# Optimization experiments

Measured on AMD Instinct MI355X. Metric: run time of the kernel, lower is better.

The kernel has to match this reference:

```python
import jax, jax.numpy as jnp
import numpy as np
from jax import lax

B, C, H0, W0 = 8, 128, 62, 62
G, K, DIL, STRIDE, PAD = 4, 3, 1, 1, 1
P = K * K
GC = C // G
OFFSET_SCALE = 1.0


def setup_inputs() -> dict:
    key = jax.random.key(0)
    ks = jax.random.split(key, 10)
    s = 0.05
    return {
        "x": jax.random.normal(ks[0], (B, C, H0, W0), jnp.float32),
        "conv_w": jax.random.normal(ks[1], (C, C, 1, 1), jnp.float32) * s,
        "conv_b": jax.random.normal(ks[2], (C,), jnp.float32) * s,
        "in_proj_w": jax.random.normal(ks[3], (C, C), jnp.float32) * s,
        "in_proj_b": jnp.zeros((C,), jnp.float32),
        "dw_w": jax.random.normal(ks[4], (C, 1, K, K), jnp.float32) * s,
        "dw_b": jnp.zeros((C,), jnp.float32),
        "ln_g": jnp.ones((C,), jnp.float32),
        "ln_b": jnp.zeros((C,), jnp.float32),
        "off_w": jax.random.normal(ks[5], (C, G * P * 2), jnp.float32) * s,
        "off_b": jax.random.normal(ks[6], (G * P * 2,), jnp.float32) * s,
        "mask_w": jax.random.normal(ks[7], (C, G * P), jnp.float32) * s,
        "mask_b": jnp.zeros((G * P,), jnp.float32),
        "out_proj_w": jax.random.normal(ks[8], (C, C), jnp.float32) * s,
        "out_proj_b": jnp.zeros((C,), jnp.float32),
    }


def _bilinear_sample(img, ix, iy, Hp, Wp):
    # img: [B, G, Hp*Wp, GC] flattened spatial; ix, iy: [B, G, Q, P] pixel coords.
    # Matches torch grid_sample(bilinear, zeros, align_corners=False).
    x0 = jnp.floor(ix)
    y0 = jnp.floor(iy)

    def gather(xi, yi):
        valid = (xi >= 0) & (xi <= Wp - 1) & (yi >= 0) & (yi <= Hp - 1)
        xc = jnp.clip(xi, 0, Wp - 1).astype(jnp.int32)
        yc = jnp.clip(yi, 0, Hp - 1).astype(jnp.int32)
        lin = (yc * Wp + xc).reshape(img.shape[0], img.shape[1], -1)  # [B,G,Q*P]
        v = jnp.take_along_axis(img, lin[..., None], axis=2)          # [B,G,Q*P,GC]
        v = v.reshape(xi.shape + (img.shape[-1],))
        return v * valid[..., None].astype(img.dtype)

    wx1 = (ix - x0)[..., None]
    wx0 = 1.0 - wx1
    wy1 = (iy - y0)[..., None]
    wy0 = 1.0 - wy1
    return (gather(x0, y0) * wx0 * wy0
            + gather(x0 + 1.0, y0) * wx1 * wy0
            + gather(x0, y0 + 1.0) * wx0 * wy1
            + gather(x0 + 1.0, y0 + 1.0) * wx1 * wy1)


def _dcnv3_core(x_proj, offset, mask):
    # x_proj: [B,H,W,C] NHWC; offset: [B,H,W,G*P*2]; mask: [B,H,W,G*P] (softmaxed)
    Bn, H, W, _ = x_proj.shape
    xp = jnp.pad(x_proj, ((0, 0), (PAD, PAD), (PAD, PAD), (0, 0)))
    Hp, Wp = H + 2 * PAD, W + 2 * PAD  # H_out == H for K=3, PAD=1, STRIDE=1
    # reference points (normalized to padded size)
    ref_x = (jnp.arange(W, dtype=jnp.float32) * STRIDE + (DIL * (K - 1)) / 2.0 + 0.5) / Wp
    ref_y = (jnp.arange(H, dtype=jnp.float32) * STRIDE + (DIL * (K - 1)) / 2.0 + 0.5) / Hp
    ref = jnp.stack(jnp.broadcast_arrays(ref_x[None, :], ref_y[:, None]), -1)  # [H,W,2] (x,y)
    # dilation grid (same ordering as torch.meshgrid(x_lin, y_lin))
    klin = (jnp.arange(K, dtype=jnp.float32) * DIL - (DIL * (K - 1)) // 2)
    gx, gy = jnp.meshgrid(klin, klin, indexing='ij')
    grid = jnp.stack([gx / Wp, gy / Hp], -1).reshape(P, 2)
    grid = jnp.tile(grid[None], (G, 1, 1)).reshape(G * P, 2)
    spatial_norm = jnp.array([Wp, Hp], jnp.float32)
    loc = (ref[:, :, None, :] + grid[None, None] * OFFSET_SCALE)[None] \
        + offset.reshape(Bn, H, W, G * P, 2) * OFFSET_SCALE / spatial_norm
    g = 2.0 * loc - 1.0  # normalized grid in [-1,1]
    ix = ((g[..., 0] + 1.0) * Wp - 1.0) / 2.0  # align_corners=False unnormalize
    iy = ((g[..., 1] + 1.0) * Hp - 1.0) / 2.0
    Q = H * W
    ix = ix.reshape(Bn, Q, G, P).transpose(0, 2, 1, 3)  # [B,G,Q,P]
    iy = iy.reshape(Bn, Q, G, P).transpose(0, 2, 1, 3)
    img = xp.reshape(Bn, Hp * Wp, G, GC).transpose(0, 2, 1, 3)  # [B,G,S,GC]
    sampled = _bilinear_sample(img, ix, iy, Hp, Wp)             # [B,G,Q,P,GC]
    m = mask.reshape(Bn, Q, G, P).transpose(0, 2, 1, 3)
    out = jnp.einsum('bgqpc,bgqp->bqgc', sampled, m)
    return out.reshape(Bn, H, W, G * GC)


def reference(x, conv_w, conv_b, in_proj_w, in_proj_b, dw_w, dw_b, ln_g, ln_b,
              off_w, off_b, mask_w, mask_b, out_proj_w, out_proj_b):
    dn = ('NCHW', 'OIHW', 'NCHW')
    # 1x1 conv with padding=1 (spatial grows by 2 on each dim)
    y = lax.conv_general_dilated(x, conv_w, (1, 1), ((PAD, PAD), (PAD, PAD)),
                                 dimension_numbers=dn) + conv_b[None, :, None, None]
    t = y.transpose(0, 2, 3, 1)  # NHWC
    x_proj = t @ in_proj_w + in_proj_b
    # offset/mask branch: depthwise conv + LayerNorm + GELU
    d = lax.conv_general_dilated(y, dw_w, (1, 1), ((1, 1), (1, 1)),
                                 dimension_numbers=dn,
                                 feature_group_count=C) + dw_b[None, :, None, None]
    d = d.transpose(0, 2, 3, 1)
    mu = d.mean(-1, keepdims=True)
    var = ((d - mu) ** 2).mean(-1, keepdims=True)
    d = (d - mu) / jnp.sqrt(var + 1e-5) * ln_g + ln_b
    d = jax.nn.gelu(d, approximate=False)
    offset = d @ off_w + off_b
    Bn, H, W, _ = d.shape
    m = jax.nn.softmax((d @ mask_w + mask_b).reshape(Bn, H, W, G, P), axis=-1)
    out = _dcnv3_core(x_proj, offset, m.reshape(Bn, H, W, G * P))
    out = out @ out_proj_w + out_proj_b
    return out.transpose(0, 3, 1, 2)  # back to NCHW
```

## Files before the change

kernel.cpp:

```cpp
#include <hip/hip_runtime.h>
#include <math.h>

#define BB 8
#define CH 128
#define HH 64
#define WWID 64
#define HIN 62
#define WIN 62
#define SPIN (HIN*WIN)
#define HP 66
#define WP 66
#define GP2 70
#define GG 4
#define GCH 32
#define NPIX (BB*HH*WWID)
#define ASTRIDE 136
#define XPHALFS ((size_t)BB*GP2*GP2*CH)

typedef _Float16 v8h __attribute__((ext_vector_type(8)));
typedef _Float16 v4h __attribute__((ext_vector_type(4)));
typedef float    v4f __attribute__((ext_vector_type(4)));
typedef float    f4a __attribute__((ext_vector_type(4), aligned(4)));

__device__ inline int xcd_swizzle(int bid, int nblk8) {
    return (bid & 7) * nblk8 + (bid >> 3);
}

__global__ __launch_bounds__(256) void p0_pack(const float* __restrict__ conv_w,
                                               const float* __restrict__ in_proj_w,
                                               const float* __restrict__ off_w,
                                               const float* __restrict__ mask_w,
                                               const float* __restrict__ out_proj_w,
                                               const float* __restrict__ dw_w,
                                               _Float16* __restrict__ wp,
                                               float* __restrict__ dwT,
                                               _Float16* __restrict__ xpad16) {
    int t = threadIdx.x;
    int blk = blockIdx.x;
    if (blk >= 32) {
        size_t nvec = XPHALFS / 8;
        for (size_t i = (size_t)(blk - 32) * 256 + t; i < nvec; i += 32 * 256)
            *(v8h*)&xpad16[i * 8] = (v8h)(_Float16)0;
        return;
    }
    if (blk == 31) {
        if (t < 128) {
            #pragma unroll
            for (int tap = 0; tap < 9; tap++) dwT[tap * 128 + t] = dw_w[t * 9 + tap];
        }
        return;
    }
    int tid = blk * 256 + t;
    int mat, base;
    if (tid < 2048)      { mat = 0; base = 0; }
    else if (tid < 4096) { mat = 1; base = 2048; }
    else if (tid < 5888) { mat = 2; base = 4096; }
    else                 { mat = 3; base = 5888; }
    int fi = tid - base;
    int nt = fi >> 8, rem = fi & 255, kc = rem >> 6, lane = rem & 63;
    int n = nt * 16 + (lane & 15);
    int kbase = kc * 32 + ((lane >> 4) & 3) * 8;
    _Float16* dst = wp + (size_t)tid * 8;
    #pragma unroll
    for (int j = 0; j < 8; j++) {
        int k = kbase + j;
        float v;
        if (mat == 0)      v = conv_w[n * CH + k];
        else if (mat == 1) v = in_proj_w[k * CH + n];
        else if (mat == 2) v = (n < 72) ? off_w[k * 72 + n]
                               : (n < 108 ? mask_w[k * 36 + (n - 72)] : 0.f);
        else               v = out_proj_w[k * CH + n];
        dst[j] = (_Float16)v;
    }
}

__device__ inline void mfma_loop8(const _Float16* __restrict__ a16,
                                  const _Float16* __restrict__ wp,
                                  v4f acc[4], int t) {
    int lane = t & 63;
    int wv = t >> 6;
    int mt = wv >> 1, ntb = (wv & 1) * 4;
    const _Float16* abase = a16 + (mt * 16 + (lane & 15)) * ASTRIDE + ((lane >> 4) * 8);
    #pragma unroll
    for (int kc = 0; kc < 4; kc++) {
        v8h av = *(const v8h*)(abase + kc * 32);
        #pragma unroll
        for (int j = 0; j < 4; j++) {
            v8h bv = *(const v8h*)(wp + ((size_t)((ntb + j) * 4 + kc) * 64 + lane) * 8);
            acc[j] = __builtin_amdgcn_mfma_f32_16x16x32_f16(av, bv, acc[j], 0, 0, 0);
        }
    }
}

__device__ inline void acc_to_a16_8(_Float16* a16, v4f acc[4], int t) {
    int lane = t & 63, ncol = lane & 15;
    int wv = t >> 6;
    int m0 = (wv >> 1) * 16 + ((lane >> 4) * 4);
    int ntb = (wv & 1) * 4;
    #pragma unroll
    for (int j = 0; j < 4; j++)
        #pragma unroll
        for (int r = 0; r < 4; r++)
            a16[(m0 + r) * ASTRIDE + (ntb + j) * 16 + ncol] = (_Float16)acc[j][r];
}

__global__ __launch_bounds__(256) void gA_conv_inproj(const float* __restrict__ x,
                                                      const _Float16* __restrict__ wp_conv,
                                                      const _Float16* __restrict__ wp_in,
                                                      const float* __restrict__ conv_b,
                                                      const float* __restrict__ in_b,
                                                      _Float16* __restrict__ y16,
                                                      _Float16* __restrict__ xpad16) {
    __shared__ _Float16 a16[32 * ASTRIDE];
    int eff = xcd_swizzle(blockIdx.x, 128);
    int pix0 = eff * 32;
    int t = threadIdx.x;
    int h = (pix0 >> 6) & 63, b = pix0 >> 12, wb = pix0 & 63;
    bool hin = (h >= 1 && h <= 62);
    for (int q = t; q < 1024; q += 256) {
        int c = q >> 3, w4l = (q & 7) * 4;
        int w4 = wb + w4l;
        float4 v = make_float4(0.f, 0.f, 0.f, 0.f);
        if (hin) {
            const float* xr = x + ((size_t)(b * CH + c)) * SPIN + (h - 1) * WIN;
            if (w4 == 0)       { f4a e = *(const f4a*)&xr[0];      v = make_float4(0.f, e[0], e[1], e[2]); }
            else if (w4 == 60) { f4a e = *(const f4a*)&xr[58];     v = make_float4(e[1], e[2], e[3], 0.f); }
            else               { f4a e = *(const f4a*)&xr[w4 - 1]; v = make_float4(e[0], e[1], e[2], e[3]); }
        }
        a16[(w4l + 0) * ASTRIDE + c] = (_Float16)v.x;
        a16[(w4l + 1) * ASTRIDE + c] = (_Float16)v.y;
        a16[(w4l + 2) * ASTRIDE + c] = (_Float16)v.z;
        a16[(w4l + 3) * ASTRIDE + c] = (_Float16)v.w;
    }
    __syncthreads();
    int lane = t & 63, ncol = lane & 15;
    int ntb = ((t >> 6) & 1) * 4;
    v4f acc[4];
    #pragma unroll
    for (int j = 0; j < 4; j++) {
        float bv = conv_b[(ntb + j) * 16 + ncol];
        acc[j] = (v4f){bv, bv, bv, bv};
    }
    mfma_loop8(a16, wp_conv, acc, t);
    __syncthreads();
    acc_to_a16_8(a16, acc, t);
    __syncthreads();
    {
        _Float16* dst = y16 + (size_t)pix0 * CH;
        for (int q = t; q < 512; q += 256)
            *(v8h*)&dst[q * 8] = *(const v8h*)&a16[(q >> 4) * ASTRIDE + (q & 15) * 8];
    }
    v4f acc2[4];
    #pragma unroll
    for (int j = 0; j < 4; j++) {
        float bv = in_b[(ntb + j) * 16 + ncol];
        acc2[j] = (v4f){bv, bv, bv, bv};
    }
    mfma_loop8(a16, wp_in, acc2, t);
    __syncthreads();
    acc_to_a16_8(a16, acc2, t);
    __syncthreads();
    {
        _Float16* dst = xpad16 + (size_t)(((b * GP2) + h + 3) * GP2 + 3 + wb) * CH;
        for (int q = t; q < 512; q += 256)
            *(v8h*)&dst[q * 8] = *(const v8h*)&a16[(q >> 4) * ASTRIDE + (q & 15) * 8];
    }
}

__global__ __launch_bounds__(512) void gF_dwln_offmask(const _Float16* __restrict__ y16,
                                                       const _Float16* __restrict__ wp_om,
                                                       const float* __restrict__ dwT,
                                                       const float* __restrict__ dw_b,
                                                       const float* __restrict__ ln_g,
                                                       const float* __restrict__ ln_b,
                                                       const float* __restrict__ off_b,
                                                       const float* __restrict__ mask_b,
                                                       float* __restrict__ tapmeta) {
    __shared__ char smem[49920];
    _Float16* ylds = (_Float16*)smem;
    int t = threadIdx.x;
    int eff = xcd_swizzle(blockIdx.x, 64);
    int pix0 = eff * 64;
    int h = (pix0 >> 6) & 63, b = pix0 >> 12;
    if (h == 0 || h == 63) {
        for (int i = t; i < 3120; i += 512) *(v8h*)&ylds[i * 8] = (v8h)(_Float16)0;
        __syncthreads();
    }
    for (int idx = t; idx < 3072; idx += 512) {
        int r = idx >> 10, w = (idx >> 4) & 63, c8 = idx & 15;
        int hh = h + r - 1;
        if (hh >= 0 && hh <= 63) {
            v8h v = *(const v8h*)&y16[(size_t)(((b * 64 + hh) * 64 + w) * CH) + c8 * 8];
            *(v8h*)&ylds[(size_t)((r * 16 + c8) * 65 + w) * 8] = v;
        }
    }
    __syncthreads();
    int px = t >> 3, q8 = t & 7;
    float acc[16];
    #pragma unroll
    for (int cb = 0; cb < 4; cb++) *(float4*)&acc[cb * 4] = *(const float4*)&dw_b[q8 * 16 + cb * 4];
    #pragma unroll
    for (int r = 0; r < 3; r++) {
        #pragma unroll
        for (int kx = 0; kx < 3; kx++) {
            int wq = px + kx - 1;
            bool valid = (wq >= 0 && wq <= 63);
            int wpc = min(max(wq, 0), 63);
            int tap = r * 3 + kx;
            if (valid) {
                #pragma unroll
                for (int cb = 0; cb < 2; cb++) {
                    v8h yv = *(const v8h*)&ylds[(size_t)((r * 16 + q8 * 2 + cb) * 65 + wpc) * 8];
                    float4 wa = *(const float4*)&dwT[tap * 128 + q8 * 16 + cb * 8];
                    float4 wb = *(const float4*)&dwT[tap * 128 + q8 * 16 + cb * 8 + 4];
                    acc[cb*8+0] += (float)yv[0] * wa.x; acc[cb*8+1] += (float)yv[1] * wa.y;
                    acc[cb*8+2] += (float)yv[2] * wa.z; acc[cb*8+3] += (float)yv[3] * wa.w;
                    acc[cb*8+4] += (float)yv[4] * wb.x; acc[cb*8+5] += (float)yv[5] * wb.y;
                    acc[cb*8+6] += (float)yv[6] * wb.z; acc[cb*8+7] += (float)yv[7] * wb.w;
                }
            }
        }
    }
    float s = 0.f, ss = 0.f;
    #pragma unroll
    for (int j = 0; j < 16; j++) { s += acc[j]; ss += acc[j] * acc[j]; }
    s  += __shfl_xor(s, 1);  s  += __shfl_xor(s, 2);  s  += __shfl_xor(s, 4);
    ss += __shfl_xor(ss, 1); ss += __shfl_xor(ss, 2); ss += __shfl_xor(ss, 4);
    float mu = s * (1.f / 128.f);
    float var = ss * (1.f / 128.f) - mu * mu;
    float rstd = rsqrtf(var + 1e-5f);
    v8h dreg[2];
    #pragma unroll
    for (int cb = 0; cb < 2; cb++) {
        float4 ga = *(const float4*)&ln_g[q8 * 16 + cb * 8];
        float4 gb = *(const float4*)&ln_g[q8 * 16 + cb * 8 + 4];
        float4 ba = *(const float4*)&ln_b[q8 * 16 + cb * 8];
        float4 bb = *(const float4*)&ln_b[q8 * 16 + cb * 8 + 4];
        float gv[8] = {ga.x, ga.y, ga.z, ga.w, gb.x, gb.y, gb.z, gb.w};
        float bv[8] = {ba.x, ba.y, ba.z, ba.w, bb.x, bb.y, bb.z, bb.w};
        #pragma unroll
        for (int j = 0; j < 8; j++) {
            float xln = (acc[cb * 8 + j] - mu) * rstd * gv[j] + bv[j];
            float gel = 0.5f * xln * (1.f + erff(xln * 0.70710678118654752f));
            dreg[cb][j] = (_Float16)gel;
        }
    }
    __syncthreads();
    _Float16* a16 = (_Float16*)smem;
    float* om = (float*)(smem + 17408);
    #pragma unroll
    for (int cb = 0; cb < 2; cb++)
        *(v8h*)&a16[px * ASTRIDE + q8 * 16 + cb * 8] = dreg[cb];
    __syncthreads();
    int lane = t & 63, ncol = lane & 15;
    int ntb = ((t >> 6) & 1) * 4;
    v4f macc[4];
    #pragma unroll
    for (int j = 0; j < 4; j++) {
        int n = (ntb + j) * 16 + ncol;
        float bv = (n < 72) ? off_b[n] : (n < 108 ? mask_b[n - 72] : 0.f);
        macc[j] = (v4f){bv, bv, bv, bv};
    }
    mfma_loop8(a16, wp_om, macc, t);
    int m0 = ((t >> 6) >> 1) * 16 + ((lane >> 4) * 4);
    #pragma unroll
    for (int j = 0; j < 4; j++) {
        if (ntb + j < 7) {
            #pragma unroll
            for (int r = 0; r < 4; r++)
                om[(m0 + r) * 112 + (ntb + j) * 16 + ncol] = macc[j][r];
        }
    }
    __syncthreads();
    {
        int job = t >> 1, half = t & 1;
        int pxs = job >> 2, gx = job & 3;
        const float* row = &om[pxs * 112];
        float lg[9];
        #pragma unroll
        for (int i = 0; i < 9; i++) lg[i] = row[72 + gx * 9 + i];
        float mx = lg[0];
        #pragma unroll
        for (int i = 1; i < 9; i++) mx = fmaxf(mx, lg[i]);
        float e[9], sum = 0.f;
        #pragma unroll
        for (int i = 0; i < 9; i++) { e[i] = expf(lg[i] - mx); sum += e[i]; }
        float inv = 1.f / sum;
        float* tm = tapmeta + ((size_t)(pix0 + pxs) * 36 + gx * 9) * 4;
        int pstart = half * 5;
        int pcount = half ? 4 : 5;
        #pragma unroll
        for (int pp = 0; pp < 5; pp++) {
            if (pp >= pcount) break;
            int p = pstart + pp;
            int gp = gx * 9 + p;
            float offx = row[gp * 2];
            float offy = row[gp * 2 + 1];
            float m = e[p] * inv;
            float ix = (float)(pxs + (p / 3)) + offx;
            float iy = (float)(h + (p % 3)) + offy;
            ix = fminf(fmaxf(ix, -2.f), (float)(WP + 1));
            iy = fminf(fmaxf(iy, -2.f), (float)(HP + 1));
            float x0f = floorf(ix), y0f = floorf(iy);
            float fx = ix - x0f, fy = iy - y0f;
            int x0 = (int)x0f, y0 = (int)y0f;
            int off = ((y0 + 2) * GP2 + (x0 + 2)) * CH;
            float4 rec;
            rec.x = __int_as_float(off);
            rec.y = fx; rec.z = fy; rec.w = m;
            *(float4*)&tm[p * 4] = rec;
        }
    }
}

__global__ __launch_bounds__(256) void kD_gather(const _Float16* __restrict__ xpad16,
                                                 const float* __restrict__ tapmeta,
                                                 _Float16* __restrict__ core16) {
    __shared__ float meta[16 * 36 * 4];
    int t = threadIdx.x;
    int eff = xcd_swizzle(blockIdx.x, 256);
    int pix0 = eff * 16;
    const float4* src = (const float4*)(tapmeta + (size_t)pix0 * 36 * 4);
    for (int i = t; i < 576; i += 256) ((float4*)meta)[i] = src[i];
    __syncthreads();
    int px_l = t >> 4, s = t & 15;
    int ch = s * 8, g = s >> 2;
    int pix = pix0 + px_l;
    int b = pix >> 12;
    const _Float16* base = xpad16 + (size_t)b * GP2 * GP2 * CH + ch;
    const float* tmb = &meta[(size_t)(px_l * 36 + g * 9) * 4];
    float acc[8];
    #pragma unroll
    for (int j = 0; j < 8; j++) acc[j] = 0.f;
    #pragma unroll
    for (int p = 0; p < 9; p++) {
        float4 rec = *(const float4*)&tmb[p * 4];
        int off = __float_as_int(rec.x);
        float fx = rec.y, fy = rec.z, m = rec.w;
        float w11 = fx * fy;
        float w10 = fx - w11;
        float w01 = fy - w11;
        float w00 = 1.f - fx - fy + w11;
        w00 *= m; w10 *= m; w01 *= m; w11 *= m;
        v8h h0 = *(const v8h*)&base[off];
        v8h h1 = *(const v8h*)&base[off + CH];
        v8h h2 = *(const v8h*)&base[off + GP2 * CH];
        v8h h3 = *(const v8h*)&base[off + GP2 * CH + CH];
        #pragma unroll
        for (int j = 0; j < 8; j++)
            acc[j] += w00*(float)h0[j] + w10*(float)h1[j] + w01*(float)h2[j] + w11*(float)h3[j];
    }
    v8h res;
    #pragma unroll
    for (int j = 0; j < 8; j++) res[j] = (_Float16)acc[j];
    *(v8h*)&core16[(size_t)pix * CH + ch] = res;
}

__global__ __launch_bounds__(512) void g4_outproj(const _Float16* __restrict__ core16,
                                                  const _Float16* __restrict__ wp,
                                                  const float* __restrict__ bias,
                                                  float* __restrict__ out) {
    __shared__ _Float16 a16[64 * ASTRIDE];
    __shared__ float res[128 * 68];
    int t = threadIdx.x;
    int eff = xcd_swizzle(blockIdx.x, 64);
    int pix0 = eff * 64;
    const _Float16* src = core16 + (size_t)pix0 * CH;
    for (int q = t; q < 1024; q += 512)
        *(v8h*)&a16[(q >> 4) * ASTRIDE + (q & 15) * 8] = *(const v8h*)&src[q * 8];
    __syncthreads();
    int lane = t & 63, ncol = lane & 15;
    int ntb = ((t >> 6) & 1) * 4;
    v4f acc[4];
    #pragma unroll
    for (int j = 0; j < 4; j++) {
        float bv = bias[(ntb + j) * 16 + ncol];
        acc[j] = (v4f){bv, bv, bv, bv};
    }
    mfma_loop8(a16, wp, acc, t);
    int m0 = ((t >> 6) >> 1) * 16 + ((lane >> 4) * 4);
    #pragma unroll
    for (int j = 0; j < 4; j++)
        #pragma unroll
        for (int r = 0; r < 4; r++)
            res[((ntb + j) * 16 + ncol) * 68 + (m0 + r)] = acc[j][r];
    __syncthreads();
    int b = pix0 >> 12, h = (pix0 >> 6) & 63;
    for (int q = t; q < 2048; q += 512) {
        int cc = q >> 4, w4 = (q & 15) * 4;
        float4 o = *(const float4*)&res[cc * 68 + w4];
        *(float4*)&out[(size_t)((b * CH + cc) * HH + h) * WWID + w4] = o;
    }
}

extern "C" void kernel_launch(void* const* d_in, const int* in_sizes, int n_in,
                              void* d_out, int out_size, void* d_ws, size_t ws_size,
                              hipStream_t stream) {
    const float* x        = (const float*)d_in[0];
    const float* conv_w   = (const float*)d_in[1];
    const float* conv_b   = (const float*)d_in[2];
    const float* in_proj_w= (const float*)d_in[3];
    const float* in_proj_b= (const float*)d_in[4];
    const float* dw_w     = (const float*)d_in[5];
    const float* dw_b     = (const float*)d_in[6];
    const float* ln_g     = (const float*)d_in[7];
    const float* ln_b     = (const float*)d_in[8];
    const float* off_w    = (const float*)d_in[9];
    const float* off_b    = (const float*)d_in[10];
    const float* mask_w   = (const float*)d_in[11];
    const float* mask_b   = (const float*)d_in[12];
    const float* out_proj_w = (const float*)d_in[13];
    const float* out_proj_b = (const float*)d_in[14];
    float* out = (float*)d_out;

    float* ws = (float*)d_ws;
    const size_t O_WP   = 0;
    const size_t O_DWT  = 32768;
    const size_t O_Y16  = 34816;
    const size_t O_XP16 = O_Y16 + 2097152;
    const size_t O_C16  = O_XP16 + 2508800;
    const size_t O_TM   = O_C16 + 2097152;
    _Float16* wp     = (_Float16*)(ws + O_WP);
    float*    dwT    = ws + O_DWT;
    _Float16* y16    = (_Float16*)(ws + O_Y16);
    _Float16* xpad16 = (_Float16*)(ws + O_XP16);
    _Float16* core16 = (_Float16*)(ws + O_C16);
    float*    tapmeta= ws + O_TM;

    _Float16* wp_conv = wp;
    _Float16* wp_in   = wp + (size_t)2048 * 8;
    _Float16* wp_om   = wp + (size_t)4096 * 8;
    _Float16* wp_out  = wp + (size_t)5888 * 8;

    p0_pack<<<64, 256, 0, stream>>>(conv_w, in_proj_w, off_w, mask_w, out_proj_w, dw_w, wp, dwT, xpad16);
    gA_conv_inproj<<<NPIX / 32, 256, 0, stream>>>(x, wp_conv, wp_in, conv_b, in_proj_b, y16, xpad16);
    gF_dwln_offmask<<<NPIX / 64, 512, 0, stream>>>(y16, wp_om, dwT, dw_b, ln_g, ln_b, off_b, mask_b, tapmeta);
    kD_gather<<<NPIX / 16, 256, 0, stream>>>(xpad16, tapmeta, core16);
    g4_outproj<<<NPIX / 64, 512, 0, stream>>>(core16, wp_out, out_proj_b, out);
}
```

Baseline: 158.8 us.

## Fuse offset/mask, deformable gather and output projection into one kernel

Merges the depthwise+LN+offset/mask kernel, the bilinear gather kernel and the out-projection kernel into a single kernel. Sampling metadata and the gathered core activations now stay in shared memory and registers instead of round-tripping through global tapmeta and core16 buffers. This also removes two kernel launches. In exchange, each thread now handles 16 channels over 9 taps with more registers, and the gather gets less parallelism per block (64 pixels per 512 threads instead of 16 per 256), which may reduce latency hiding for the random gathers.

```diff
diff --git a/kernel.cpp b/kernel.cpp
--- a/kernel.cpp
+++ b/kernel.cpp
@@ -11,14 +11,11 @@
 #define HP 66
 #define WP 66
 #define GP2 70
-#define GG 4
-#define GCH 32
 #define NPIX (BB*HH*WWID)
 #define ASTRIDE 136
 #define XPHALFS ((size_t)BB*GP2*GP2*CH)
 
 typedef _Float16 v8h __attribute__((ext_vector_type(8)));
-typedef _Float16 v4h __attribute__((ext_vector_type(4)));
 typedef float    v4f __attribute__((ext_vector_type(4)));
 typedef float    f4a __attribute__((ext_vector_type(4), aligned(4)));
 
@@ -167,15 +164,18 @@
     }
 }
 
-__global__ __launch_bounds__(512) void gF_dwln_offmask(const _Float16* __restrict__ y16,
-                                                       const _Float16* __restrict__ wp_om,
-                                                       const float* __restrict__ dwT,
-                                                       const float* __restrict__ dw_b,
-                                                       const float* __restrict__ ln_g,
-                                                       const float* __restrict__ ln_b,
-                                                       const float* __restrict__ off_b,
-                                                       const float* __restrict__ mask_b,
-                                                       float* __restrict__ tapmeta) {
+__global__ __launch_bounds__(512) void gF_mega(const _Float16* __restrict__ y16,
+                                               const _Float16* __restrict__ xpad16,
+                                               const _Float16* __restrict__ wp_om,
+                                               const _Float16* __restrict__ wp_out,
+                                               const float* __restrict__ dwT,
+                                               const float* __restrict__ dw_b,
+                                               const float* __restrict__ ln_g,
+                                               const float* __restrict__ ln_b,
+                                               const float* __restrict__ off_b,
+                                               const float* __restrict__ mask_b,
+                                               const float* __restrict__ out_b,
+                                               float* __restrict__ out) {
     __shared__ char smem[49920];
     _Float16* ylds = (_Float16*)smem;
     int t = threadIdx.x;
@@ -211,12 +211,12 @@
                 #pragma unroll
                 for (int cb = 0; cb < 2; cb++) {
                     v8h yv = *(const v8h*)&ylds[(size_t)((r * 16 + q8 * 2 + cb) * 65 + wpc) * 8];
-                    float4 wa = *(const float4*)&dwT[tap * 128 + q8 * 16 + cb * 8];
-                    float4 wb = *(const float4*)&dwT[tap * 128 + q8 * 16 + cb * 8 + 4];
-                    acc[cb*8+0] += (float)yv[0] * wa.x; acc[cb*8+1] += (float)yv[1] * wa.y;
-                    acc[cb*8+2] += (float)yv[2] * wa.z; acc[cb*8+3] += (float)yv[3] * wa.w;
-                    acc[cb*8+4] += (float)yv[4] * wb.x; acc[cb*8+5] += (float)yv[5] * wb.y;
-                    acc[cb*8+6] += (float)yv[6] * wb.z; acc[cb*8+7] += (float)yv[7] * wb.w;
+                    float4 wa  = *(const float4*)&dwT[tap * 128 + q8 * 16 + cb * 8];
+                    float4 wbv = *(const float4*)&dwT[tap * 128 + q8 * 16 + cb * 8 + 4];
+                    acc[cb*8+0] += (float)yv[0] * wa.x;  acc[cb*8+1] += (float)yv[1] * wa.y;
+                    acc[cb*8+2] += (float)yv[2] * wa.z;  acc[cb*8+3] += (float)yv[3] * wa.w;
+                    acc[cb*8+4] += (float)yv[4] * wbv.x; acc[cb*8+5] += (float)yv[5] * wbv.y;
+                    acc[cb*8+6] += (float)yv[6] * wbv.z; acc[cb*8+7] += (float)yv[7] * wbv.w;
                 }
             }
         }
@@ -254,31 +254,35 @@
     __syncthreads();
     int lane = t & 63, ncol = lane & 15;
     int ntb = ((t >> 6) & 1) * 4;
-    v4f macc[4];
-    #pragma unroll
-    for (int j = 0; j < 4; j++) {
-        int n = (ntb + j) * 16 + ncol;
-        float bv = (n < 72) ? off_b[n] : (n < 108 ? mask_b[n - 72] : 0.f);
-        macc[j] = (v4f){bv, bv, bv, bv};
-    }
-    mfma_loop8(a16, wp_om, macc, t);
-    int m0 = ((t >> 6) >> 1) * 16 + ((lane >> 4) * 4);
-    #pragma unroll
-    for (int j = 0; j < 4; j++) {
-        if (ntb + j < 7) {
-            #pragma unroll
-            for (int r = 0; r < 4; r++)
-                om[(m0 + r) * 112 + (ntb + j) * 16 + ncol] = macc[j][r];
-        }
-    }
-    __syncthreads();
     {
-        int job = t >> 1, half = t & 1;
-        int pxs = job >> 2, gx = job & 3;
-        const float* row = &om[pxs * 112];
+        v4f macc[4];
+        #pragma unroll
+        for (int j = 0; j < 4; j++) {
+            int n = (ntb + j) * 16 + ncol;
+            float bv = (n < 72) ? off_b[n] : (n < 108 ? mask_b[n - 72] : 0.f);
+            macc[j] = (v4f){bv, bv, bv, bv};
+        }
+        mfma_loop8(a16, wp_om, macc, t);
+        int m0 = ((t >> 6) >> 1) * 16 + ((lane >> 4) * 4);
+        #pragma unroll
+        for (int j = 0; j < 4; j++) {
+            if (ntb + j < 7) {
+                #pragma unroll
+                for (int r = 0; r < 4; r++)
+                    om[(m0 + r) * 112 + (ntb + j) * 16 + ncol] = macc[j][r];
+            }
+        }
+    }
+    __syncthreads();
+    {
+        int s8 = t & 7;
+        int ch = s8 * 16, g = s8 >> 1;
+        g = s8 >> 1;
+        g = s8 >> 1;
+        const float* row = &om[px * 112];
         float lg[9];
         #pragma unroll
-        for (int i = 0; i < 9; i++) lg[i] = row[72 + gx * 9 + i];
+        for (int i = 0; i < 9; i++) lg[i] = row[72 + g * 9 + i];
         float mx = lg[0];
         #pragma unroll
         for (int i = 1; i < 9; i++) mx = fmaxf(mx, lg[i]);
@@ -286,18 +290,16 @@
         #pragma unroll
         for (int i = 0; i < 9; i++) { e[i] = expf(lg[i] - mx); sum += e[i]; }
         float inv = 1.f / sum;
-        float* tm = tapmeta + ((size_t)(pix0 + pxs) * 36 + gx * 9) * 4;
-        int pstart = half * 5;
-        int pcount = half ? 4 : 5;
-        #pragma unroll
-        for (int pp = 0; pp < 5; pp++) {
-            if (pp >= pcount) break;
-            int p = pstart + pp;
-            int gp = gx * 9 + p;
-            float offx = row[gp * 2];
-            float offy = row[gp * 2 + 1];
+        const _Float16* base = xpad16 + (size_t)b * GP2 * GP2 * CH + ch;
+        float gacc[16];
+        #pragma unroll
+        for (int j = 0; j < 16; j++) gacc[j] = 0.f;
+        #pragma unroll
+        for (int p = 0; p < 9; p++) {
+            float offx = row[(g * 9 + p) * 2];
+            float offy = row[(g * 9 + p) * 2 + 1];
             float m = e[p] * inv;
-            float ix = (float)(pxs + (p / 3)) + offx;
+            float ix = (float)(px + (p / 3)) + offx;
             float iy = (float)(h + (p % 3)) + offy;
             ix = fminf(fmaxf(ix, -2.f), (float)(WP + 1));
             iy = fminf(fmaxf(iy, -2.f), (float)(HP + 1));
@@ -305,91 +307,55 @@
             float fx = ix - x0f, fy = iy - y0f;
             int x0 = (int)x0f, y0 = (int)y0f;
             int off = ((y0 + 2) * GP2 + (x0 + 2)) * CH;
-            float4 rec;
-            rec.x = __int_as_float(off);
-            rec.y = fx; rec.z = fy; rec.w = m;
-            *(float4*)&tm[p * 4] = rec;
-        }
-    }
-}
-
-__global__ __launch_bounds__(256) void kD_gather(const _Float16* __restrict__ xpad16,
-                                                 const float* __restrict__ tapmeta,
-                                                 _Float16* __restrict__ core16) {
-    __shared__ float meta[16 * 36 * 4];
-    int t = threadIdx.x;
-    int eff = xcd_swizzle(blockIdx.x, 256);
-    int pix0 = eff * 16;
-    const float4* src = (const float4*)(tapmeta + (size_t)pix0 * 36 * 4);
-    for (int i = t; i < 576; i += 256) ((float4*)meta)[i] = src[i];
-    __syncthreads();
-    int px_l = t >> 4, s = t & 15;
-    int ch = s * 8, g = s >> 2;
-    int pix = pix0 + px_l;
-    int b = pix >> 12;
-    const _Float16* base = xpad16 + (size_t)b * GP2 * GP2 * CH + ch;
-    const float* tmb = &meta[(size_t)(px_l * 36 + g * 9) * 4];
-    float acc[8];
-    #pragma unroll
-    for (int j = 0; j < 8; j++) acc[j] = 0.f;
-    #pragma unroll
-    for (int p = 0; p < 9; p++) {
-        float4 rec = *(const float4*)&tmb[p * 4];
-        int off = __float_as_int(rec.x);
-        float fx = rec.y, fy = rec.z, m = rec.w;
-        float w11 = fx * fy;
-        float w10 = fx - w11;
-        float w01 = fy - w11;
-        float w00 = 1.f - fx - fy + w11;
-        w00 *= m; w10 *= m; w01 *= m; w11 *= m;
-        v8h h0 = *(const v8h*)&base[off];
-        v8h h1 = *(const v8h*)&base[off + CH];
-        v8h h2 = *(const v8h*)&base[off + GP2 * CH];
-        v8h h3 = *(const v8h*)&base[off + GP2 * CH + CH];
-        #pragma unroll
-        for (int j = 0; j < 8; j++)
-            acc[j] += w00*(float)h0[j] + w10*(float)h1[j] + w01*(float)h2[j] + w11*(float)h3[j];
-    }
-    v8h res;
-    #pragma unroll
-    for (int j = 0; j < 8; j++) res[j] = (_Float16)acc[j];
-    *(v8h*)&core16[(size_t)pix * CH + ch] = res;
-}
-
-__global__ __launch_bounds__(512) void g4_outproj(const _Float16* __restrict__ core16,
-                                                  const _Float16* __restrict__ wp,
-                                                  const float* __restrict__ bias,
-                                                  float* __restrict__ out) {
-    __shared__ _Float16 a16[64 * ASTRIDE];
-    __shared__ float res[128 * 68];
-    int t = threadIdx.x;
-    int eff = xcd_swizzle(blockIdx.x, 64);
-    int pix0 = eff * 64;
-    const _Float16* src = core16 + (size_t)pix0 * CH;
-    for (int q = t; q < 1024; q += 512)
-        *(v8h*)&a16[(q >> 4) * ASTRIDE + (q & 15) * 8] = *(const v8h*)&src[q * 8];
-    __syncthreads();
-    int lane = t & 63, ncol = lane & 15;
-    int ntb = ((t >> 6) & 1) * 4;
-    v4f acc[4];
-    #pragma unroll
-    for (int j = 0; j < 4; j++) {
-        float bv = bias[(ntb + j) * 16 + ncol];
-        acc[j] = (v4f){bv, bv, bv, bv};
-    }
-    mfma_loop8(a16, wp, acc, t);
-    int m0 = ((t >> 6) >> 1) * 16 + ((lane >> 4) * 4);
-    #pragma unroll
-    for (int j = 0; j < 4; j++)
-        #pragma unroll
-        for (int r = 0; r < 4; r++)
-            res[((ntb + j) * 16 + ncol) * 68 + (m0 + r)] = acc[j][r];
-    __syncthreads();
-    int b = pix0 >> 12, h = (pix0 >> 6) & 63;
-    for (int q = t; q < 2048; q += 512) {
-        int cc = q >> 4, w4 = (q & 15) * 4;
-        float4 o = *(const float4*)&res[cc * 68 + w4];
-        *(float4*)&out[(size_t)((b * CH + cc) * HH + h) * WWID + w4] = o;
+            float w11 = fx * fy;
+            float w10 = fx - w11;
+            float w01 = fy - w11;
+            float w00 = 1.f - fx - fy + w11;
+            w00 *= m; w10 *= m; w01 *= m; w11 *= m;
+            v8h c0a = *(const v8h*)&base[off];
+            v8h c0b = *(const v8h*)&base[off + 8];
+            v8h c1a = *(const v8h*)&base[off + CH];
+            v8h c1b = *(const v8h*)&base[off + CH + 8];
+            v8h c2a = *(const v8h*)&base[off + GP2 * CH];
+            v8h c2b = *(const v8h*)&base[off + GP2 * CH + 8];
+            v8h c3a = *(const v8h*)&base[off + GP2 * CH + CH];
+            v8h c3b = *(const v8h*)&base[off + GP2 * CH + CH + 8];
+            #pragma unroll
+            for (int j = 0; j < 8; j++) {
+                gacc[j]     += w00*(float)c0a[j] + w10*(float)c1a[j] + w01*(float)c2a[j] + w11*(float)c3a[j];
+                gacc[j + 8] += w00*(float)c0b[j] + w10*(float)c1b[j] + w01*(float)c2b[j] + w11*(float)c3b[j];
+            }
+        }
+        __syncthreads();
+        v8h r0, r1;
+        #pragma unroll
+        for (int j = 0; j < 8; j++) { r0[j] = (_Float16)gacc[j]; r1[j] = (_Float16)gacc[j + 8]; }
+        *(v8h*)&a16[px * ASTRIDE + ch]     = r0;
+        *(v8h*)&a16[px * ASTRIDE + ch + 8] = r1;
+    }
+    __syncthreads();
+    {
+        v4f oacc[4];
+        #pragma unroll
+        for (int j = 0; j < 4; j++) {
+            float bv = out_b[(ntb + j) * 16 + ncol];
+            oacc[j] = (v4f){bv, bv, bv, bv};
+        }
+        mfma_loop8(a16, wp_out, oacc, t);
+        __syncthreads();
+        float* res = (float*)smem;
+        int m0 = ((t >> 6) >> 1) * 16 + ((lane >> 4) * 4);
+        #pragma unroll
+        for (int j = 0; j < 4; j++)
+            #pragma unroll
+            for (int r = 0; r < 4; r++)
+                res[((ntb + j) * 16 + ncol) * 68 + (m0 + r)] = oacc[j][r];
+        __syncthreads();
+        for (int q = t; q < 2048; q += 512) {
+            int cc = q >> 4, w4 = (q & 15) * 4;
+            float4 o = *(const float4*)&res[cc * 68 + w4];
+            *(float4*)&out[(size_t)((b * CH + cc) * HH + h) * WWID + w4] = o;
+        }
     }
 }
 
@@ -418,14 +384,10 @@
     const size_t O_DWT  = 32768;
     const size_t O_Y16  = 34816;
     const size_t O_XP16 = O_Y16 + 2097152;
-    const size_t O_C16  = O_XP16 + 2508800;
-    const size_t O_TM   = O_C16 + 2097152;
     _Float16* wp     = (_Float16*)(ws + O_WP);
     float*    dwT    = ws + O_DWT;
     _Float16* y16    = (_Float16*)(ws + O_Y16);
     _Float16* xpad16 = (_Float16*)(ws + O_XP16);
-    _Float16* core16 = (_Float16*)(ws + O_C16);
-    float*    tapmeta= ws + O_TM;
 
     _Float16* wp_conv = wp;
     _Float16* wp_in   = wp + (size_t)2048 * 8;
@@ -434,7 +396,6 @@
 
     p0_pack<<<64, 256, 0, stream>>>(conv_w, in_proj_w, off_w, mask_w, out_proj_w, dw_w, wp, dwT, xpad16);
     gA_conv_inproj<<<NPIX / 32, 256, 0, stream>>>(x, wp_conv, wp_in, conv_b, in_proj_b, y16, xpad16);
-    gF_dwln_offmask<<<NPIX / 64, 512, 0, stream>>>(y16, wp_om, dwT, dw_b, ln_g, ln_b, off_b, mask_b, tapmeta);
-    kD_gather<<<NPIX / 16, 256, 0, stream>>>(xpad16, tapmeta, core16);
-    g4_outproj<<<NPIX / 64, 512, 0, stream>>>(core16, wp_out, out_proj_b, out);
-}
+    gF_mega<<<NPIX / 64, 512, 0, stream>>>(y16, xpad16, wp_om, wp_out, dwT, dw_b,
+                                           ln_g, ln_b, off_b, mask_b, out_proj_b, out);
+}
```

Result: slower. 211.2 us (+33.0%).
